# Performance work log

Hardware: AMD Instinct MI355X
Metric: run time of the kernel (lower is better)

## Reference

```python
import jax, jax.numpy as jnp
import numpy as np

HEADS = 8
DIM_HEAD = 64
EPS = 1e-5


def _inst_norm_lastdim(t):
    # torch InstanceNorm1d receives [(b h), n, d]; with affine=False it normalizes
    # over the spatial (last) dim d per (b,h,n), biased variance, eps=1e-5.
    mu = jnp.mean(t, axis=-1, keepdims=True)
    var = jnp.mean(jnp.square(t - mu), axis=-1, keepdims=True)
    return (t - mu) * jax.lax.rsqrt(var + EPS)


def setup_inputs() -> dict:
    key = jax.random.key(0)
    k1, k2, k3, k4 = jax.random.split(key, 4)
    b, n, dim = 4, 8192, 256
    inner = HEADS * DIM_HEAD  # 512
    x = jax.random.normal(k1, (b, n, dim), dtype=jnp.float32)
    Wqkv = jax.random.normal(k2, (3 * inner, dim), dtype=jnp.float32) * (1.0 / np.sqrt(dim))
    Wout = jax.random.normal(k3, (dim, inner), dtype=jnp.float32) * (1.0 / np.sqrt(inner))
    bout = jax.random.normal(k4, (dim,), dtype=jnp.float32) * 0.01
    return {"x": x, "Wqkv": Wqkv, "Wout": Wout, "bout": bout}


def reference(x, Wqkv, Wout, bout):
    b, n, dim = x.shape
    qkv = jnp.einsum('bnc,fc->bnf', x, Wqkv)  # [b, n, 3*inner]
    q, k, v = jnp.split(qkv, 3, axis=-1)
    def to_heads(t):
        return t.reshape(b, n, HEADS, DIM_HEAD).transpose(0, 2, 1, 3)  # [b,h,n,d]
    q, k, v = to_heads(q), to_heads(k), to_heads(v)
    # galerkin: instance-norm k and v
    k = _inst_norm_lastdim(k)
    v = _inst_norm_lastdim(v)
    # associative linear attention: (k^T v) then q @ dots, scaled by 1/n
    dots = jnp.einsum('bhnd,bhne->bhde', k, v)        # [b,h,d,d]
    out = jnp.einsum('bhnd,bhde->bhne', q, dots) / n  # [b,h,n,d]
    out = out.transpose(0, 2, 1, 3).reshape(b, n, HEADS * DIM_HEAD)
    return jnp.einsum('bnf,cf->bnc', out, Wout) + bout
```

## Files before the change

### kernel.cpp

```cpp
#include <hip/hip_runtime.h>
#include <hip/hip_bf16.h>

#define SEQ    8192
#define NROWS  32768
#define F3     1536
#define EPS    1e-5f

typedef __attribute__((ext_vector_type(4))) float f32x4;
typedef __attribute__((ext_vector_type(8))) short bf16x8;
typedef __attribute__((ext_vector_type(8))) unsigned short u16x8;

__device__ __forceinline__ unsigned short f2bu(float f) {
  __hip_bfloat16 h = __float2bfloat16(f);
  return __builtin_bit_cast(unsigned short, h);
}
__device__ __forceinline__ float b2f(unsigned short u) {
  return __bfloat162float(__builtin_bit_cast(__hip_bfloat16, u));
}

__global__ __launch_bounds__(256) void convert_kernel(const float* __restrict__ in,
                                                      unsigned short* __restrict__ out, int n4) {
  int i = blockIdx.x * 256 + threadIdx.x;
  if (i >= n4) return;
  float4 v = reinterpret_cast<const float4*>(in)[i];
  ushort4 o;
  o.x = f2bu(v.x); o.y = f2bu(v.y); o.z = f2bu(v.z); o.w = f2bu(v.w);
  reinterpret_cast<ushort4*>(out)[i] = o;
}

template<int K, int LDA, int LDC, bool PERB, bool BIAS, bool OUTF32>
__global__ __launch_bounds__(256) void gemm_kernel(const unsigned short* __restrict__ A,
                                                   const unsigned short* __restrict__ Bw,
                                                   const float* __restrict__ bias,
                                                   void* __restrict__ Cout) {
  __shared__ unsigned short As[128 * 64];
  __shared__ unsigned short Bs[128 * 64];
  const int row0 = blockIdx.x * 128;
  const int col0 = blockIdx.y * 128;
  const unsigned short* Bp = Bw;
  if constexpr (PERB) Bp += (size_t)(row0 >> 13) * (size_t)(LDC * K);
  const int tid  = threadIdx.x;
  const int lane = tid & 63;
  const int wave = tid >> 6;
  const int wr = (wave >> 1) << 6;
  const int wc = (wave & 1) << 6;
  const int srow = tid >> 3;
  const int scol = (tid & 7) << 3;

  f32x4 acc[4][4] = {};

  for (int k0 = 0; k0 < K; k0 += 64) {
#pragma unroll
    for (int it = 0; it < 4; ++it) {
      const unsigned short* ga = A + (size_t)(row0 + it * 32 + srow) * LDA + (k0 + scol);
      __builtin_amdgcn_global_load_lds(
          (const __attribute__((address_space(1))) void*)ga,
          (__attribute__((address_space(3))) void*)((char*)As + (it * 4096 + wave * 1024)),
          16, 0, 0);
      const unsigned short* gb = Bp + (size_t)(col0 + it * 32 + srow) * K + (k0 + scol);
      __builtin_amdgcn_global_load_lds(
          (const __attribute__((address_space(1))) void*)gb,
          (__attribute__((address_space(3))) void*)((char*)Bs + (it * 4096 + wave * 1024)),
          16, 0, 0);
    }
    __syncthreads();
#pragma unroll
    for (int ks = 0; ks < 2; ++ks) {
      bf16x8 af[4], bfr[4];
#pragma unroll
      for (int mt = 0; mt < 4; ++mt)
        af[mt] = *reinterpret_cast<const bf16x8*>(
            &As[(wr + mt * 16 + (lane & 15)) * 64 + ks * 32 + (lane >> 4) * 8]);
#pragma unroll
      for (int nt = 0; nt < 4; ++nt)
        bfr[nt] = *reinterpret_cast<const bf16x8*>(
            &Bs[(wc + nt * 16 + (lane & 15)) * 64 + ks * 32 + (lane >> 4) * 8]);
#pragma unroll
      for (int mt = 0; mt < 4; ++mt)
#pragma unroll
        for (int nt = 0; nt < 4; ++nt)
          acc[mt][nt] = __builtin_amdgcn_mfma_f32_16x16x32_bf16(af[mt], bfr[nt], acc[mt][nt], 0, 0, 0);
    }
    __syncthreads();
  }
#pragma unroll
  for (int mt = 0; mt < 4; ++mt) {
#pragma unroll
    for (int nt = 0; nt < 4; ++nt) {
      const int col = col0 + wc + nt * 16 + (lane & 15);
      float bv = 0.0f;
      if constexpr (BIAS) bv = bias[col];
#pragma unroll
      for (int i = 0; i < 4; ++i) {
        const int row = row0 + wr + mt * 16 + ((lane >> 4) << 2) + i;
        float v = acc[mt][nt][i] + bv;
        if constexpr (OUTF32)
          reinterpret_cast<float*>(Cout)[(size_t)row * LDC + col] = v;
        else
          reinterpret_cast<unsigned short*>(Cout)[(size_t)row * LDC + col] = f2bu(v);
      }
    }
  }
}

__global__ __launch_bounds__(256) void dots_kernel(const unsigned short* __restrict__ qkv,
                                                   float* __restrict__ partial) {
  const int bh = blockIdx.x;
  const int chunk = blockIdx.y;
  const int b = bh >> 3, h = bh & 7;
  const int t = threadIdx.x;
  __shared__ float lbuf[2][4360];

  const int r  = t >> 3;
  const int j  = t & 7;
  const int kv = j >> 2;
  const int jj = j & 3;
  const int dq = t & 15;
  const int eq = t >> 4;

  const size_t rowbase = (size_t)(b * SEQ + chunk * 512 + r) * F3 + 512 + kv * 512 + h * 64 + jj * 16;
  const int lds_off = kv * 2180 + r * 68 + jj * 16;

  float acc[4][4] = {};
  u16x8 raw0, raw1;
  raw0 = *reinterpret_cast<const u16x8*>(qkv + rowbase);
  raw1 = *reinterpret_cast<const u16x8*>(qkv + rowbase + 8);

  int p = 0;
  {
    float x[16];
#pragma unroll
    for (int i = 0; i < 8; ++i) { x[i] = b2f(raw0[i]); x[8 + i] = b2f(raw1[i]); }
    float s = 0.f, s2 = 0.f;
#pragma unroll
    for (int i = 0; i < 16; ++i) { s += x[i]; s2 += x[i] * x[i]; }
    s += __shfl_xor(s, 1, 64);  s2 += __shfl_xor(s2, 1, 64);
    s += __shfl_xor(s, 2, 64);  s2 += __shfl_xor(s2, 2, 64);
    const float mean = s * (1.0f / 64.0f);
    float var = s2 * (1.0f / 64.0f) - mean * mean;
    var = var < 0.f ? 0.f : var;
    const float rs = rsqrtf(var + EPS);
    float* dst = &lbuf[0][lds_off];
#pragma unroll
    for (int i = 0; i < 4; ++i) {
      f32x4 o = { (x[4*i+0]-mean)*rs, (x[4*i+1]-mean)*rs, (x[4*i+2]-mean)*rs, (x[4*i+3]-mean)*rs };
      *reinterpret_cast<f32x4*>(dst + 4 * i) = o;
    }
  }

  for (int sIt = 0; sIt < 16; ++sIt) {
    const bool more = (sIt + 1) < 16;
    if (more) {
      const unsigned short* src = qkv + rowbase + (size_t)(sIt + 1) * 32 * F3;
      raw0 = *reinterpret_cast<const u16x8*>(src);
      raw1 = *reinterpret_cast<const u16x8*>(src + 8);
    }
    __syncthreads();
    {
      const float* lk = &lbuf[p][0];
      const float* lv = &lbuf[p][2180];
#pragma unroll 4
      for (int rr = 0; rr < 32; ++rr) {
        f32x4 kf = *reinterpret_cast<const f32x4*>(lk + rr * 68 + dq * 4);
        f32x4 vf = *reinterpret_cast<const f32x4*>(lv + rr * 68 + eq * 4);
#pragma unroll
        for (int i = 0; i < 4; ++i)
#pragma unroll
          for (int jx = 0; jx < 4; ++jx)
            acc[i][jx] = fmaf(kf[i], vf[jx], acc[i][jx]);
      }
    }
    if (more) {
      float x[16];
#pragma unroll
      for (int i = 0; i < 8; ++i) { x[i] = b2f(raw0[i]); x[8 + i] = b2f(raw1[i]); }
      float s = 0.f, s2 = 0.f;
#pragma unroll
      for (int i = 0; i < 16; ++i) { s += x[i]; s2 += x[i] * x[i]; }
      s += __shfl_xor(s, 1, 64);  s2 += __shfl_xor(s2, 1, 64);
      s += __shfl_xor(s, 2, 64);  s2 += __shfl_xor(s2, 2, 64);
      const float mean = s * (1.0f / 64.0f);
      float var = s2 * (1.0f / 64.0f) - mean * mean;
      var = var < 0.f ? 0.f : var;
      const float rs = rsqrtf(var + EPS);
      float* dst = &lbuf[p ^ 1][lds_off];
#pragma unroll
      for (int i = 0; i < 4; ++i) {
        f32x4 o = { (x[4*i+0]-mean)*rs, (x[4*i+1]-mean)*rs, (x[4*i+2]-mean)*rs, (x[4*i+3]-mean)*rs };
        *reinterpret_cast<f32x4*>(dst + 4 * i) = o;
      }
    }
    p ^= 1;
  }

  float* pp = partial + ((size_t)(chunk * 32 + bh) << 12) + (size_t)(dq * 4) * 64 + eq * 4;
#pragma unroll
  for (int i = 0; i < 4; ++i) {
    f32x4 o = { acc[i][0], acc[i][1], acc[i][2], acc[i][3] };
    *reinterpret_cast<f32x4*>(pp + i * 64) = o;
  }
}

__global__ __launch_bounds__(256) void reduce_kernel(const float* __restrict__ partial,
                                                     float* __restrict__ dots) {
  const int i = blockIdx.x * 256 + threadIdx.x;
  f32x4 s = {};
#pragma unroll
  for (int c = 0; c < 16; ++c)
    s += reinterpret_cast<const f32x4*>(partial)[(size_t)c * 32768 + i];
  reinterpret_cast<f32x4*>(dots)[i] = s;
}

__global__ __launch_bounds__(512) void m2_kernel(const float* __restrict__ dots,
                                                 const float* __restrict__ Wout,
                                                 unsigned short* __restrict__ M2) {
  const int b = blockIdx.x;
  const int c = blockIdx.y;
  const int t = threadIdx.x;
  __shared__ float wrow[512];
  wrow[t] = Wout[(size_t)c * 512 + t];
  __syncthreads();
  const int h = t >> 6, d = t & 63;
  const float* dp = dots + (size_t)(b * 8 + h) * 4096 + (size_t)d * 64;
  float s = 0.0f;
#pragma unroll 8
  for (int e = 0; e < 64; ++e) s += dp[e] * wrow[(h << 6) + e];
  M2[((size_t)b * 256 + c) * 512 + t] = f2bu(s * (1.0f / 8192.0f));
}

extern "C" void kernel_launch(void* const* d_in, const int* in_sizes, int n_in,
                              void* d_out, int out_size, void* d_ws, size_t ws_size,
                              hipStream_t stream) {
  const float* x    = (const float*)d_in[0];
  const float* Wqkv = (const float*)d_in[1];
  const float* Wout = (const float*)d_in[2];
  const float* bout = (const float*)d_in[3];
  char* ws = (char*)d_ws;
  unsigned short* xb    = (unsigned short*)(ws);
  float*          part  = (float*)         (ws);
  unsigned short* wqkvb = (unsigned short*)(ws + 16777216);
  unsigned short* qkvb  = (unsigned short*)(ws + 17563648);
  float*          dots  = (float*)         (ws + 118226944);
  unsigned short* m2    = (unsigned short*)(ws + 118751232);

  convert_kernel<<<dim3(8192), 256, 0, stream>>>(x, xb, 2097152);
  convert_kernel<<<dim3(384), 256, 0, stream>>>(Wqkv, wqkvb, 98304);
  gemm_kernel<256, 256, 1536, false, false, false><<<dim3(256, 12), 256, 0, stream>>>(xb, wqkvb, nullptr, qkvb);
  dots_kernel<<<dim3(32, 16), 256, 0, stream>>>(qkvb, part);
  reduce_kernel<<<dim3(128), 256, 0, stream>>>(part, dots);
  m2_kernel<<<dim3(4, 256), 512, 0, stream>>>(dots, Wout, m2);
  gemm_kernel<512, 1536, 256, true, true, true><<<dim3(256, 2), 256, 0, stream>>>(qkvb, m2, bout, d_out);
}
```

Baseline: 205.6 us.

## Fold Wq into per-batch output weights and skip materializing Q

Rather than computing Q through the big projection GEMM and then multiplying by M2, the change precomputes W3 = M2·Wq per batch with a small GEMM and applies it straight to x (K=256 instead of 512). Only K and V get projected and stored, which cuts the first GEMM's N from 1536 to 1024 and removes the Q write and reread. The bf16 GEMM epilogue now stages through LDS for coalesced 16-byte stores, and the grid axes are swapped. The cost is an extra transpose kernel for Wq and one more bf16 rounding stage in W3.

```diff
diff --git a/kernel.cpp b/kernel.cpp
--- a/kernel.cpp
+++ b/kernel.cpp
@@ -3,7 +3,6 @@
 
 #define SEQ    8192
 #define NROWS  32768
-#define F3     1536
 #define EPS    1e-5f
 
 typedef __attribute__((ext_vector_type(4))) float f32x4;
@@ -28,15 +27,36 @@
   reinterpret_cast<ushort4*>(out)[i] = o;
 }
 
+__global__ __launch_bounds__(256) void wprep_kernel(const float* __restrict__ W,
+                                                    unsigned short* __restrict__ wb,
+                                                    unsigned short* __restrict__ wqT) {
+  int i = blockIdx.x * 256 + threadIdx.x;
+  if (i >= 98304) return;
+  float4 v = reinterpret_cast<const float4*>(W)[i];
+  ushort4 o;
+  o.x = f2bu(v.x); o.y = f2bu(v.y); o.z = f2bu(v.z); o.w = f2bu(v.w);
+  reinterpret_cast<ushort4*>(wb)[i] = o;
+  const int e = i * 4;
+  const int f = e >> 8;
+  if (f < 512) {
+    const int c = e & 255;
+    wqT[(size_t)(c + 0) * 512 + f] = o.x;
+    wqT[(size_t)(c + 1) * 512 + f] = o.y;
+    wqT[(size_t)(c + 2) * 512 + f] = o.z;
+    wqT[(size_t)(c + 3) * 512 + f] = o.w;
+  }
+}
+
 template<int K, int LDA, int LDC, bool PERB, bool BIAS, bool OUTF32>
 __global__ __launch_bounds__(256) void gemm_kernel(const unsigned short* __restrict__ A,
                                                    const unsigned short* __restrict__ Bw,
                                                    const float* __restrict__ bias,
                                                    void* __restrict__ Cout) {
-  __shared__ unsigned short As[128 * 64];
-  __shared__ unsigned short Bs[128 * 64];
-  const int row0 = blockIdx.x * 128;
-  const int col0 = blockIdx.y * 128;
+  __shared__ char smem[32768];
+  unsigned short* As = (unsigned short*)smem;
+  unsigned short* Bs = (unsigned short*)(smem + 16384);
+  const int row0 = blockIdx.y * 128;
+  const int col0 = blockIdx.x * 128;
   const unsigned short* Bp = Bw;
   if constexpr (PERB) Bp += (size_t)(row0 >> 13) * (size_t)(LDC * K);
   const int tid  = threadIdx.x;
@@ -83,27 +103,49 @@
     }
     __syncthreads();
   }
-#pragma unroll
-  for (int mt = 0; mt < 4; ++mt) {
-#pragma unroll
-    for (int nt = 0; nt < 4; ++nt) {
-      const int col = col0 + wc + nt * 16 + (lane & 15);
-      float bv = 0.0f;
-      if constexpr (BIAS) bv = bias[col];
-#pragma unroll
-      for (int i = 0; i < 4; ++i) {
-        const int row = row0 + wr + mt * 16 + ((lane >> 4) << 2) + i;
-        float v = acc[mt][nt][i] + bv;
-        if constexpr (OUTF32)
-          reinterpret_cast<float*>(Cout)[(size_t)row * LDC + col] = v;
-        else
-          reinterpret_cast<unsigned short*>(Cout)[(size_t)row * LDC + col] = f2bu(v);
-      }
-    }
-  }
-}
-
-__global__ __launch_bounds__(256) void dots_kernel(const unsigned short* __restrict__ qkv,
+
+  if constexpr (OUTF32) {
+#pragma unroll
+    for (int mt = 0; mt < 4; ++mt) {
+#pragma unroll
+      for (int nt = 0; nt < 4; ++nt) {
+        const int col = col0 + wc + nt * 16 + (lane & 15);
+        float bv = 0.0f;
+        if constexpr (BIAS) bv = bias[col];
+#pragma unroll
+        for (int i = 0; i < 4; ++i) {
+          const int row = row0 + wr + mt * 16 + ((lane >> 4) << 2) + i;
+          reinterpret_cast<float*>(Cout)[(size_t)row * LDC + col] = acc[mt][nt][i] + bv;
+        }
+      }
+    }
+  } else {
+    unsigned short* Ct = (unsigned short*)smem;
+#pragma unroll
+    for (int mt = 0; mt < 4; ++mt) {
+#pragma unroll
+      for (int nt = 0; nt < 4; ++nt) {
+        const int lc = wc + nt * 16 + (lane & 15);
+        float bv = 0.0f;
+        if constexpr (BIAS) bv = bias[col0 + lc];
+#pragma unroll
+        for (int i = 0; i < 4; ++i) {
+          const int lr = wr + mt * 16 + ((lane >> 4) << 2) + i;
+          Ct[lr * 128 + lc] = f2bu(acc[mt][nt][i] + bv);
+        }
+      }
+    }
+    __syncthreads();
+    const int r = tid >> 1, cs = (tid & 1) << 6;
+    unsigned short* gout = (unsigned short*)Cout + (size_t)(row0 + r) * LDC + col0 + cs;
+    const unsigned short* lsrc = Ct + r * 128 + cs;
+#pragma unroll
+    for (int i = 0; i < 8; ++i)
+      *reinterpret_cast<u16x8*>(gout + i * 8) = *reinterpret_cast<const u16x8*>(lsrc + i * 8);
+  }
+}
+
+__global__ __launch_bounds__(256) void dots_kernel(const unsigned short* __restrict__ kvb,
                                                    float* __restrict__ partial) {
   const int bh = blockIdx.x;
   const int chunk = blockIdx.y;
@@ -118,13 +160,13 @@
   const int dq = t & 15;
   const int eq = t >> 4;
 
-  const size_t rowbase = (size_t)(b * SEQ + chunk * 512 + r) * F3 + 512 + kv * 512 + h * 64 + jj * 16;
+  const size_t rowbase = (size_t)(b * SEQ + chunk * 512 + r) * 1024 + kv * 512 + h * 64 + jj * 16;
   const int lds_off = kv * 2180 + r * 68 + jj * 16;
 
   float acc[4][4] = {};
   u16x8 raw0, raw1;
-  raw0 = *reinterpret_cast<const u16x8*>(qkv + rowbase);
-  raw1 = *reinterpret_cast<const u16x8*>(qkv + rowbase + 8);
+  raw0 = *reinterpret_cast<const u16x8*>(kvb + rowbase);
+  raw1 = *reinterpret_cast<const u16x8*>(kvb + rowbase + 8);
 
   int p = 0;
   {
@@ -151,7 +193,7 @@
   for (int sIt = 0; sIt < 16; ++sIt) {
     const bool more = (sIt + 1) < 16;
     if (more) {
-      const unsigned short* src = qkv + rowbase + (size_t)(sIt + 1) * 32 * F3;
+      const unsigned short* src = kvb + rowbase + (size_t)(sIt + 1) * 32 * 1024;
       raw0 = *reinterpret_cast<const u16x8*>(src);
       raw1 = *reinterpret_cast<const u16x8*>(src + 8);
     }
@@ -237,17 +279,21 @@
   const float* bout = (const float*)d_in[3];
   char* ws = (char*)d_ws;
   unsigned short* xb    = (unsigned short*)(ws);
-  float*          part  = (float*)         (ws);
   unsigned short* wqkvb = (unsigned short*)(ws + 16777216);
-  unsigned short* qkvb  = (unsigned short*)(ws + 17563648);
-  float*          dots  = (float*)         (ws + 118226944);
-  unsigned short* m2    = (unsigned short*)(ws + 118751232);
+  unsigned short* wqT   = (unsigned short*)(ws + 17563648);
+  unsigned short* kvb   = (unsigned short*)(ws + 17825792);
+  float*          part  = (float*)         (ws + 84934656);
+  float*          dots  = (float*)         (ws + 93323264);
+  unsigned short* m2    = (unsigned short*)(ws + 93847552);
+  unsigned short* w3    = (unsigned short*)(ws + 94896128);
 
   convert_kernel<<<dim3(8192), 256, 0, stream>>>(x, xb, 2097152);
-  convert_kernel<<<dim3(384), 256, 0, stream>>>(Wqkv, wqkvb, 98304);
-  gemm_kernel<256, 256, 1536, false, false, false><<<dim3(256, 12), 256, 0, stream>>>(xb, wqkvb, nullptr, qkvb);
-  dots_kernel<<<dim3(32, 16), 256, 0, stream>>>(qkvb, part);
+  wprep_kernel<<<dim3(384), 256, 0, stream>>>(Wqkv, wqkvb, wqT);
+  gemm_kernel<256, 256, 1024, false, false, false><<<dim3(8, 256), 256, 0, stream>>>(
+      xb, wqkvb + (size_t)512 * 256, nullptr, kvb);
+  dots_kernel<<<dim3(32, 16), 256, 0, stream>>>(kvb, part);
   reduce_kernel<<<dim3(128), 256, 0, stream>>>(part, dots);
   m2_kernel<<<dim3(4, 256), 512, 0, stream>>>(dots, Wout, m2);
-  gemm_kernel<512, 1536, 256, true, true, true><<<dim3(256, 2), 256, 0, stream>>>(qkvb, m2, bout, d_out);
-}
+  gemm_kernel<512, 512, 256, false, false, false><<<dim3(2, 8), 256, 0, stream>>>(m2, wqT, nullptr, w3);
+  gemm_kernel<256, 256, 256, true, true, true><<<dim3(2, 256), 256, 0, stream>>>(xb, w3, bout, d_out);
+}
```

New measurement: 218.8 us. +6.4%, slower.
